# Optimization experiments

Measured on AMD Instinct MI355X. Metric: run time of the kernel, lower is better.

The kernel has to match this reference:

```python
import jax, jax.numpy as jnp
import numpy as np

N_NODES = 50000
N_EDGES = 800000
IN_CH = 128
HID_CH = 128


def setup_inputs() -> dict:
    key = jax.random.key(0)
    k1, k2, k3, k4 = jax.random.split(key, 4)
    x = jax.random.normal(k1, (N_NODES, IN_CH), dtype=jnp.float32)
    edge_index = jax.random.randint(k2, (2, N_EDGES), 0, N_NODES, dtype=jnp.int32)
    # Glorot-ish init for weights
    W1 = jax.random.normal(k3, (IN_CH, HID_CH), dtype=jnp.float32) / np.sqrt(IN_CH)
    b1 = jnp.zeros((HID_CH,), dtype=jnp.float32)
    W2 = jax.random.normal(k4, (HID_CH, 1), dtype=jnp.float32) / np.sqrt(HID_CH)
    b2 = jnp.zeros((1,), dtype=jnp.float32)
    return {"x": x, "edge_index": edge_index, "W1": W1, "b1": b1, "W2": W2, "b2": b2}


def gcn_conv(x, W, b, src, dst, n_nodes):
    """PyG GCNConv: add self-loops, symmetric deg normalization, linear + bias."""
    h = x @ W  # [N, out]
    # degree including self-loop (edge weights are 1)
    deg = jnp.zeros((n_nodes,), dtype=h.dtype).at[dst].add(1.0) + 1.0
    dinv = jax.lax.rsqrt(deg)  # deg >= 1, safe
    norm = dinv[src] * dinv[dst]  # [E]
    msg = h[src] * norm[:, None]  # gather + edgewise scale
    out = jax.ops.segment_sum(msg, dst, num_segments=n_nodes)
    # self-loop contribution: norm_ii = dinv[i]^2
    out = out + h * (dinv * dinv)[:, None]
    return out + b


def reference(x, edge_index, W1, b1, W2, b2):
    src, dst = edge_index[0], edge_index[1]
    n = x.shape[0]
    z = jax.nn.relu(gcn_conv(x, W1, b1, src, dst, n))
    z = gcn_conv(z, W2, b2, src, dst, n)  # [N, 1]
    # decode: edgewise dot product + sigmoid
    logits = jnp.sum(z[src] * z[dst], axis=1)  # [E]
    return jax.nn.sigmoid(logits)
```

## Files before the change

### kernel.cpp

```cpp
#include <hip/hip_runtime.h>
#include <hip/hip_bf16.h>
#include <math.h>

#define N_NODES 50000
#define N_EDGES 800000
#define CH 128
#define WID 64
#define SH 8
#define NBKT 196
#define BCAP 5120

typedef _Float16 half2t __attribute__((ext_vector_type(2)));
typedef _Float16 half4t __attribute__((ext_vector_type(4)));
typedef _Float16 half8t __attribute__((ext_vector_type(8)));
typedef float    floatx4 __attribute__((ext_vector_type(4)));

__global__ void k_zero(int* __restrict__ gcur) {
    gcur[threadIdx.x] = 0;
}

__global__ __launch_bounds__(256) void k_bin(const int* __restrict__ src,
                                             const int* __restrict__ dst,
                                             int* __restrict__ gcur,
                                             unsigned int* __restrict__ pairs,
                                             const float* __restrict__ b1,
                                             const float* __restrict__ W2,
                                             float* __restrict__ b1p,
                                             float* __restrict__ W2p, int E) {
    __shared__ int hist[NBKT];
    __shared__ int gpos[NBKT];
    const int t = threadIdx.x;
    if (t < NBKT) hist[t] = 0;
    __syncthreads();
    const int base = blockIdx.x * 1024;
    int bb[4], rr[4];
    unsigned int vv[4];
#pragma unroll
    for (int i = 0; i < 4; ++i) {
        int e = base + i * 256 + t;
        bb[i] = -1;
        if (e < E) {
            int d = dst[e];
            bb[i] = d >> SH;
            vv[i] = (unsigned int)src[e] | ((unsigned int)(d & 255) << 16);
            rr[i] = atomicAdd(&hist[bb[i]], 1);
        }
    }
    __syncthreads();
    if (t < NBKT) {
        int c = hist[t];
        gpos[t] = (c > 0) ? atomicAdd(&gcur[t], c) : 0;
    }
    __syncthreads();
#pragma unroll
    for (int i = 0; i < 4; ++i) {
        if (bb[i] >= 0) {
            int p = gpos[bb[i]] + rr[i];
            if (p < BCAP) pairs[(size_t)bb[i] * BCAP + p] = vv[i];
        }
    }
    if (blockIdx.x == 0 && t < 128) {
        int cp = t;
        int c  = (cp & 7) * 16 + (cp >> 3);
        b1p[cp] = b1[c];
        W2p[cp] = W2[c];
    }
}

__global__ __launch_bounds__(256) void k_build(const int* __restrict__ gcur,
                                               const unsigned int* __restrict__ pairs,
                                               unsigned short* __restrict__ ell,
                                               int* __restrict__ cnt_g,
                                               float* __restrict__ dinv, int N) {
    __shared__ unsigned short ell_s[256 * WID];
    __shared__ int cnt_s[256];
    const int t = threadIdx.x, b = blockIdx.x;
    cnt_s[t] = 0;
    __syncthreads();
    const int cntb = min(gcur[b], BCAP);
    const unsigned int* pp = pairs + (size_t)b * BCAP;
    for (int j = t; j < cntb; j += 256) {
        unsigned int u = pp[j];
        int lo = u >> 16;
        int c = atomicAdd(&cnt_s[lo], 1);
        if (c < WID) ell_s[lo * WID + c] = (unsigned short)(u & 0xFFFFu);
    }
    __syncthreads();
    const unsigned int* ls = (const unsigned int*)ell_s;
    unsigned int* lg = (unsigned int*)ell + (size_t)b * (256 * WID / 2);
#pragma unroll
    for (int i = 0; i < 32; ++i) lg[t + 256 * i] = ls[t + 256 * i];
    int node = b * 256 + t;
    if (node < N) {
        cnt_g[node] = cnt_s[t];
        dinv[node]  = rsqrtf((float)cnt_s[t] + 1.0f);
    }
}

__global__ __launch_bounds__(256) void k_gemm(const float* __restrict__ x,
                                              const float* __restrict__ W,
                                              const float* __restrict__ dinv,
                                              _Float16* __restrict__ hs, int M) {
    __shared__ _Float16 Wh[32 * 128 * 4];
    const int tid = threadIdx.x;
#pragma unroll
    for (int pass = 0; pass < 16; ++pass) {
        int kg = pass * 2 + (tid >> 7);
        int n  = tid & 127;
        const float* wp = W + (kg * 4) * 128 + n;
        half4t v;
        v[0] = (_Float16)wp[0];
        v[1] = (_Float16)wp[128];
        v[2] = (_Float16)wp[256];
        v[3] = (_Float16)wp[384];
        *(half4t*)&Wh[(kg * 128 + n) * 4] = v;
    }
    __syncthreads();

    const int w    = tid >> 6;
    const int lane = tid & 63;
    const int lrow = lane & 15;
    const int lhi  = lane >> 4;
    const int arow = blockIdx.x * 64 + w * 16 + lrow;
    const bool avalid = arow < M;
    const float* xp = x + (size_t)arow * CH;

    floatx4 acc[8];
#pragma unroll
    for (int t = 0; t < 8; ++t) acc[t] = (floatx4){0.f, 0.f, 0.f, 0.f};

#pragma unroll
    for (int s = 0; s < 8; ++s) {
        floatx4 xa = (floatx4){0.f, 0.f, 0.f, 0.f};
        if (avalid) xa = *(const floatx4*)(xp + s * 16 + lhi * 4);
        half4t a;
        a[0] = (_Float16)xa[0]; a[1] = (_Float16)xa[1];
        a[2] = (_Float16)xa[2]; a[3] = (_Float16)xa[3];
        const int kg = s * 4 + lhi;
#pragma unroll
        for (int t = 0; t < 8; ++t) {
            half4t bv = *(const half4t*)&Wh[(kg * 128 + t * 16 + lrow) * 4];
            acc[t] = __builtin_amdgcn_mfma_f32_16x16x16f16(a, bv, acc[t], 0, 0, 0);
        }
    }

    const int base = blockIdx.x * 64 + w * 16 + lhi * 4;
    if (base < M) {
        floatx4 dv = *(const floatx4*)(dinv + base);
#pragma unroll
        for (int i = 0; i < 4; ++i) {
            half8t o;
#pragma unroll
            for (int t = 0; t < 8; ++t) o[t] = (_Float16)(acc[t][i] * dv[i]);
            *(half8t*)(hs + (size_t)(base + i) * CH + lrow * 8) = o;
        }
    }
}

__global__ __launch_bounds__(256) void k_agg1(const _Float16* __restrict__ hs,
                                              const float* __restrict__ dinv,
                                              const float* __restrict__ b1p,
                                              const float* __restrict__ W2p,
                                              const int* __restrict__ cnt,
                                              const unsigned short* __restrict__ ell,
                                              float* __restrict__ h2s, int N) {
    int node = blockIdx.x * 4 + (threadIdx.x >> 6);
    int lane = threadIdx.x & 63;
    if (node >= N) return;
    int deg = min(cnt[node], WID);
    int l = lane & 15;
    int q = lane >> 4;
    int idxv = (lane < deg) ? (int)ell[(size_t)node * WID + lane] : 0;

    float acc[8];
    if (q == 0) {
        half8t v = *(const half8t*)(hs + (size_t)node * CH + 8 * l);
#pragma unroll
        for (int c = 0; c < 8; ++c) acc[c] = (float)v[c];
    } else {
#pragma unroll
        for (int c = 0; c < 8; ++c) acc[c] = 0.f;
    }

    for (int j0 = q; j0 < deg; j0 += 16) {
        int j1 = j0 + 4, j2 = j0 + 8, j3 = j0 + 12;
        int s0 = __shfl(idxv, j0);
        int s1 = __shfl(idxv, j1 & 63);
        int s2 = __shfl(idxv, j2 & 63);
        int s3 = __shfl(idxv, j3 & 63);
        half8t v0 = *(const half8t*)(hs + (size_t)s0 * CH + 8 * l);
        half8t v1 = *(const half8t*)(hs + (size_t)s1 * CH + 8 * l);
        half8t v2 = *(const half8t*)(hs + (size_t)s2 * CH + 8 * l);
        half8t v3 = *(const half8t*)(hs + (size_t)s3 * CH + 8 * l);
#pragma unroll
        for (int c = 0; c < 8; ++c) acc[c] += (float)v0[c];
        if (j1 < deg) {
#pragma unroll
            for (int c = 0; c < 8; ++c) acc[c] += (float)v1[c];
        }
        if (j2 < deg) {
#pragma unroll
            for (int c = 0; c < 8; ++c) acc[c] += (float)v2[c];
        }
        if (j3 < deg) {
#pragma unroll
            for (int c = 0; c < 8; ++c) acc[c] += (float)v3[c];
        }
    }
#pragma unroll
    for (int c = 0; c < 8; ++c) {
        acc[c] += __shfl_xor(acc[c], 16);
        acc[c] += __shfl_xor(acc[c], 32);
    }

    float di = dinv[node];
    floatx4 b0 = *(const floatx4*)(b1p + 8 * l);
    floatx4 b1v = *(const floatx4*)(b1p + 8 * l + 4);
    floatx4 w0 = *(const floatx4*)(W2p + 8 * l);
    floatx4 w1 = *(const floatx4*)(W2p + 8 * l + 4);
    float a = 0.f;
#pragma unroll
    for (int c = 0; c < 4; ++c) {
        a += fmaxf(fmaf(acc[c], di, b0[c]), 0.f) * w0[c];
        a += fmaxf(fmaf(acc[c + 4], di, b1v[c]), 0.f) * w1[c];
    }
    a += __shfl_down(a, 8);
    a += __shfl_down(a, 4);
    a += __shfl_down(a, 2);
    a += __shfl_down(a, 1);
    if (lane == 0) h2s[node] = a * di;
}

__global__ __launch_bounds__(256) void k_agg2(const float* __restrict__ h2s,
                                              const float* __restrict__ dinv,
                                              const float* __restrict__ b2,
                                              const int* __restrict__ cnt,
                                              const unsigned short* __restrict__ ell,
                                              float* __restrict__ out2, int N) {
    int t = blockIdx.x * blockDim.x + threadIdx.x;
    int node = t >> 3;
    int gl = t & 7;
    if (node >= N) return;
    int deg = min(cnt[node], WID);
    float acc = 0.f;
    for (int j = gl; j < deg; j += 8)
        acc += h2s[ell[(size_t)node * WID + j]];
    acc += __shfl_xor(acc, 4);
    acc += __shfl_xor(acc, 2);
    acc += __shfl_xor(acc, 1);
    if (gl == 0) out2[node] = fmaf(acc + h2s[node], dinv[node], b2[0]);
}

__global__ void k_decode(const float* __restrict__ out2, const int* __restrict__ src,
                         const int* __restrict__ dst, float* __restrict__ out, int E) {
    int t = blockIdx.x * blockDim.x + threadIdx.x;
    int e0 = t * 4;
    if (e0 + 3 < E) {
        int4 s4 = *(const int4*)(src + e0);
        int4 d4 = *(const int4*)(dst + e0);
        float4 o;
        o.x = 1.0f / (1.0f + __expf(-out2[s4.x] * out2[d4.x]));
        o.y = 1.0f / (1.0f + __expf(-out2[s4.y] * out2[d4.y]));
        o.z = 1.0f / (1.0f + __expf(-out2[s4.z] * out2[d4.z]));
        o.w = 1.0f / (1.0f + __expf(-out2[s4.w] * out2[d4.w]));
        *(float4*)(out + e0) = o;
    } else {
        for (int e = e0; e < E; ++e) {
            float z = out2[src[e]] * out2[dst[e]];
            out[e] = 1.0f / (1.0f + __expf(-z));
        }
    }
}

extern "C" void kernel_launch(void* const* d_in, const int* in_sizes, int n_in,
                              void* d_out, int out_size, void* d_ws, size_t ws_size,
                              hipStream_t stream) {
    const float* x   = (const float*)d_in[0];
    const int*   ei  = (const int*)d_in[1];
    const float* W1  = (const float*)d_in[2];
    const float* b1  = (const float*)d_in[3];
    const float* W2  = (const float*)d_in[4];
    const float* b2  = (const float*)d_in[5];
    float* out = (float*)d_out;

    const int N = N_NODES;
    const int E = N_EDGES;
    const int* src = ei;
    const int* dst = ei + E;

    const int NP = 50176;
    float* ws    = (float*)d_ws;
    float* dinv  = ws;
    int*   cnt   = (int*)(ws + NP);
    float* h2s   = ws + 2 * NP;
    float* out2  = ws + 3 * NP;
    float* b1p   = ws + 4 * NP;
    float* W2p   = b1p + CH;
    int*   gcur  = (int*)(W2p + CH);
    unsigned int* pairs = (unsigned int*)(gcur + 256);
    unsigned short* ell = (unsigned short*)(pairs + (size_t)NBKT * BCAP);
    _Float16* hs = (_Float16*)((unsigned int*)ell + (size_t)NP * WID / 2);

    k_zero<<<1, 256, 0, stream>>>(gcur);

    k_bin<<<(E + 1023) / 1024, 256, 0, stream>>>(src, dst, gcur, pairs, b1, W2, b1p, W2p, E);
    k_build<<<NBKT, 256, 0, stream>>>(gcur, pairs, ell, cnt, dinv, N);

    k_gemm<<<(N + 63) / 64, 256, 0, stream>>>(x, W1, dinv, hs, N);

    k_agg1<<<(N + 3) / 4, 256, 0, stream>>>(hs, dinv, b1p, W2p, cnt, ell, h2s, N);
    k_agg2<<<(N * 8 + 255) / 256, 256, 0, stream>>>(h2s, dinv, b2, cnt, ell, out2, N);
    k_decode<<<(E / 4 + 255) / 256, 256, 0, stream>>>(out2, src, dst, out, E);
}
```

Before: 96.20 us.

## Split feature matrix into four channel panels and aggregate each panel separately

The GEMM now writes the fp16 hidden features as four 32-channel panels instead of row-major 128-channel rows. The first-layer aggregation runs four times, once per panel, and combines the partial second-layer dot products through a store on the first pass and atomics after that. Each panel is about 3.2 MB, so the random neighbour gathers should stay in cache. The cost is four kernel launches, reading the neighbour lists four times, and float atomics whose summation order is not fixed. Nontemporal loads and stores are also added to the one-use pair and neighbour-list buffers.

```diff
diff --git a/kernel.cpp b/kernel.cpp
--- a/kernel.cpp
+++ b/kernel.cpp
@@ -9,6 +9,8 @@
 #define SH 8
 #define NBKT 196
 #define BCAP 5120
+#define NPAD 50176
+#define PNL 32
 
 typedef _Float16 half2t __attribute__((ext_vector_type(2)));
 typedef _Float16 half4t __attribute__((ext_vector_type(4)));
@@ -56,7 +58,8 @@
     for (int i = 0; i < 4; ++i) {
         if (bb[i] >= 0) {
             int p = gpos[bb[i]] + rr[i];
-            if (p < BCAP) pairs[(size_t)bb[i] * BCAP + p] = vv[i];
+            if (p < BCAP)
+                __builtin_nontemporal_store(vv[i], pairs + (size_t)bb[i] * BCAP + p);
         }
     }
     if (blockIdx.x == 0 && t < 128) {
@@ -80,7 +83,7 @@
     const int cntb = min(gcur[b], BCAP);
     const unsigned int* pp = pairs + (size_t)b * BCAP;
     for (int j = t; j < cntb; j += 256) {
-        unsigned int u = pp[j];
+        unsigned int u = __builtin_nontemporal_load(pp + j);
         int lo = u >> 16;
         int c = atomicAdd(&cnt_s[lo], 1);
         if (c < WID) ell_s[lo * WID + c] = (unsigned short)(u & 0xFFFFu);
@@ -89,7 +92,8 @@
     const unsigned int* ls = (const unsigned int*)ell_s;
     unsigned int* lg = (unsigned int*)ell + (size_t)b * (256 * WID / 2);
 #pragma unroll
-    for (int i = 0; i < 32; ++i) lg[t + 256 * i] = ls[t + 256 * i];
+    for (int i = 0; i < 32; ++i)
+        __builtin_nontemporal_store(ls[t + 256 * i], lg + t + 256 * i);
     int node = b * 256 + t;
     if (node < N) {
         cnt_g[node] = cnt_s[t];
@@ -100,7 +104,7 @@
 __global__ __launch_bounds__(256) void k_gemm(const float* __restrict__ x,
                                               const float* __restrict__ W,
                                               const float* __restrict__ dinv,
-                                              _Float16* __restrict__ hs, int M) {
+                                              _Float16* __restrict__ hs4, int M) {
     __shared__ _Float16 Wh[32 * 128 * 4];
     const int tid = threadIdx.x;
 #pragma unroll
@@ -147,88 +151,77 @@
     const int base = blockIdx.x * 64 + w * 16 + lhi * 4;
     if (base < M) {
         floatx4 dv = *(const floatx4*)(dinv + base);
+        _Float16* hb = hs4 + (size_t)(lrow >> 2) * NPAD * PNL + (lrow & 3) * 8;
 #pragma unroll
         for (int i = 0; i < 4; ++i) {
             half8t o;
 #pragma unroll
             for (int t = 0; t < 8; ++t) o[t] = (_Float16)(acc[t][i] * dv[i]);
-            *(half8t*)(hs + (size_t)(base + i) * CH + lrow * 8) = o;
-        }
-    }
-}
-
-__global__ __launch_bounds__(256) void k_agg1(const _Float16* __restrict__ hs,
-                                              const float* __restrict__ dinv,
-                                              const float* __restrict__ b1p,
-                                              const float* __restrict__ W2p,
-                                              const int* __restrict__ cnt,
-                                              const unsigned short* __restrict__ ell,
-                                              float* __restrict__ h2s, int N) {
+            *(half8t*)(hb + (size_t)(base + i) * PNL) = o;
+        }
+    }
+}
+
+__global__ __launch_bounds__(256) void k_agg1p(const _Float16* __restrict__ hs4,
+                                               const float* __restrict__ dinv,
+                                               const float* __restrict__ b1p,
+                                               const float* __restrict__ W2p,
+                                               const int* __restrict__ cnt,
+                                               const unsigned short* __restrict__ ell,
+                                               float* __restrict__ h2s, int N,
+                                               int p, int first) {
     int node = blockIdx.x * 4 + (threadIdx.x >> 6);
     int lane = threadIdx.x & 63;
     if (node >= N) return;
     int deg = min(cnt[node], WID);
-    int l = lane & 15;
-    int q = lane >> 4;
-    int idxv = (lane < deg) ? (int)ell[(size_t)node * WID + lane] : 0;
-
-    float acc[8];
-    if (q == 0) {
-        half8t v = *(const half8t*)(hs + (size_t)node * CH + 8 * l);
-#pragma unroll
-        for (int c = 0; c < 8; ++c) acc[c] = (float)v[c];
-    } else {
-#pragma unroll
-        for (int c = 0; c < 8; ++c) acc[c] = 0.f;
-    }
-
-    for (int j0 = q; j0 < deg; j0 += 16) {
-        int j1 = j0 + 4, j2 = j0 + 8, j3 = j0 + 12;
+    int l = lane & 7;
+    int o = lane >> 3;
+    int idxv = (lane < deg)
+        ? (int)__builtin_nontemporal_load(ell + (size_t)node * WID + lane) : 0;
+    const _Float16* hsp = hs4 + (size_t)p * NPAD * PNL;
+
+    float acc[4] = {0.f, 0.f, 0.f, 0.f};
+    if (o == 0) {
+        half4t v = *(const half4t*)(hsp + (size_t)node * PNL + 4 * l);
+#pragma unroll
+        for (int c = 0; c < 4; ++c) acc[c] = (float)v[c];
+    }
+
+    for (int j0 = o; j0 < deg; j0 += 16) {
+        int j1 = j0 + 8;
         int s0 = __shfl(idxv, j0);
         int s1 = __shfl(idxv, j1 & 63);
-        int s2 = __shfl(idxv, j2 & 63);
-        int s3 = __shfl(idxv, j3 & 63);
-        half8t v0 = *(const half8t*)(hs + (size_t)s0 * CH + 8 * l);
-        half8t v1 = *(const half8t*)(hs + (size_t)s1 * CH + 8 * l);
-        half8t v2 = *(const half8t*)(hs + (size_t)s2 * CH + 8 * l);
-        half8t v3 = *(const half8t*)(hs + (size_t)s3 * CH + 8 * l);
-#pragma unroll
-        for (int c = 0; c < 8; ++c) acc[c] += (float)v0[c];
+        half4t v0 = *(const half4t*)(hsp + (size_t)s0 * PNL + 4 * l);
+        half4t v1 = *(const half4t*)(hsp + (size_t)s1 * PNL + 4 * l);
+#pragma unroll
+        for (int c = 0; c < 4; ++c) acc[c] += (float)v0[c];
         if (j1 < deg) {
 #pragma unroll
-            for (int c = 0; c < 8; ++c) acc[c] += (float)v1[c];
-        }
-        if (j2 < deg) {
-#pragma unroll
-            for (int c = 0; c < 8; ++c) acc[c] += (float)v2[c];
-        }
-        if (j3 < deg) {
-#pragma unroll
-            for (int c = 0; c < 8; ++c) acc[c] += (float)v3[c];
-        }
-    }
-#pragma unroll
-    for (int c = 0; c < 8; ++c) {
+            for (int c = 0; c < 4; ++c) acc[c] += (float)v1[c];
+        }
+    }
+#pragma unroll
+    for (int c = 0; c < 4; ++c) {
+        acc[c] += __shfl_xor(acc[c], 8);
         acc[c] += __shfl_xor(acc[c], 16);
         acc[c] += __shfl_xor(acc[c], 32);
     }
 
     float di = dinv[node];
-    floatx4 b0 = *(const floatx4*)(b1p + 8 * l);
-    floatx4 b1v = *(const floatx4*)(b1p + 8 * l + 4);
-    floatx4 w0 = *(const floatx4*)(W2p + 8 * l);
-    floatx4 w1 = *(const floatx4*)(W2p + 8 * l + 4);
+    floatx4 bv = *(const floatx4*)(b1p + p * PNL + 4 * l);
+    floatx4 wv = *(const floatx4*)(W2p + p * PNL + 4 * l);
     float a = 0.f;
 #pragma unroll
-    for (int c = 0; c < 4; ++c) {
-        a += fmaxf(fmaf(acc[c], di, b0[c]), 0.f) * w0[c];
-        a += fmaxf(fmaf(acc[c + 4], di, b1v[c]), 0.f) * w1[c];
-    }
-    a += __shfl_down(a, 8);
+    for (int c = 0; c < 4; ++c)
+        a += fmaxf(fmaf(acc[c], di, bv[c]), 0.f) * wv[c];
     a += __shfl_down(a, 4);
     a += __shfl_down(a, 2);
     a += __shfl_down(a, 1);
-    if (lane == 0) h2s[node] = a * di;
+    if (lane == 0) {
+        float v = a * di;
+        if (first) h2s[node] = v;
+        else       atomicAdd(&h2s[node], v);
+    }
 }
 
 __global__ __launch_bounds__(256) void k_agg2(const float* __restrict__ h2s,
@@ -244,7 +237,7 @@
     int deg = min(cnt[node], WID);
     float acc = 0.f;
     for (int j = gl; j < deg; j += 8)
-        acc += h2s[ell[(size_t)node * WID + j]];
+        acc += h2s[__builtin_nontemporal_load(ell + (size_t)node * WID + j)];
     acc += __shfl_xor(acc, 4);
     acc += __shfl_xor(acc, 2);
     acc += __shfl_xor(acc, 1);
@@ -288,27 +281,28 @@
     const int* src = ei;
     const int* dst = ei + E;
 
-    const int NP = 50176;
     float* ws    = (float*)d_ws;
     float* dinv  = ws;
-    int*   cnt   = (int*)(ws + NP);
-    float* h2s   = ws + 2 * NP;
-    float* out2  = ws + 3 * NP;
-    float* b1p   = ws + 4 * NP;
+    int*   cnt   = (int*)(ws + NPAD);
+    float* h2s   = ws + 2 * NPAD;
+    float* out2  = ws + 3 * NPAD;
+    float* b1p   = ws + 4 * NPAD;
     float* W2p   = b1p + CH;
     int*   gcur  = (int*)(W2p + CH);
     unsigned int* pairs = (unsigned int*)(gcur + 256);
     unsigned short* ell = (unsigned short*)(pairs + (size_t)NBKT * BCAP);
-    _Float16* hs = (_Float16*)((unsigned int*)ell + (size_t)NP * WID / 2);
+    _Float16* hs4 = (_Float16*)((unsigned int*)ell + (size_t)NPAD * WID / 2);
 
     k_zero<<<1, 256, 0, stream>>>(gcur);
 
     k_bin<<<(E + 1023) / 1024, 256, 0, stream>>>(src, dst, gcur, pairs, b1, W2, b1p, W2p, E);
     k_build<<<NBKT, 256, 0, stream>>>(gcur, pairs, ell, cnt, dinv, N);
 
-    k_gemm<<<(N + 63) / 64, 256, 0, stream>>>(x, W1, dinv, hs, N);
-
-    k_agg1<<<(N + 3) / 4, 256, 0, stream>>>(hs, dinv, b1p, W2p, cnt, ell, h2s, N);
+    k_gemm<<<(N + 63) / 64, 256, 0, stream>>>(x, W1, dinv, hs4, N);
+
+    for (int p = 0; p < 4; ++p)
+        k_agg1p<<<(N + 3) / 4, 256, 0, stream>>>(hs4, dinv, b1p, W2p, cnt, ell,
+                                                 h2s, N, p, p == 0 ? 1 : 0);
     k_agg2<<<(N * 8 + 255) / 256, 256, 0, stream>>>(h2s, dinv, b2, cnt, ell, out2, N);
     k_decode<<<(E / 4 + 255) / 256, 256, 0, stream>>>(out2, src, dst, out, E);
 }
```

After: 176.0 us. 1.83x slower.

## Store hidden features as FP8 and gather 16 channels per lane in aggregation

Applied to the files above, without the earlier changes.

The GEMM epilogue now packs the dinv-scaled hidden features into FP8 with cvt_pk_fp8 instead of FP16. This halves the bytes per row that the edge gather in the first aggregation reads. The aggregation kernel is restructured so each lane loads 16 bytes (16 channels) per neighbor, with 8 neighbor slots per wave and an extra shuffle reduction step. The binning kernel also switches to contiguous int4 loads of src and dst. The cost is a large drop in precision for the intermediate features, which risks accuracy against the reference.

```diff
diff --git a/kernel.cpp b/kernel.cpp
--- a/kernel.cpp
+++ b/kernel.cpp
@@ -10,10 +10,10 @@
 #define NBKT 196
 #define BCAP 5120
 
-typedef _Float16 half2t __attribute__((ext_vector_type(2)));
 typedef _Float16 half4t __attribute__((ext_vector_type(4)));
 typedef _Float16 half8t __attribute__((ext_vector_type(8)));
 typedef float    floatx4 __attribute__((ext_vector_type(4)));
+typedef float    floatx2 __attribute__((ext_vector_type(2)));
 
 __global__ void k_zero(int* __restrict__ gcur) {
     gcur[threadIdx.x] = 0;
@@ -32,18 +32,31 @@
     const int t = threadIdx.x;
     if (t < NBKT) hist[t] = 0;
     __syncthreads();
-    const int base = blockIdx.x * 1024;
+    const int e0 = blockIdx.x * 1024 + t * 4;
     int bb[4], rr[4];
     unsigned int vv[4];
-#pragma unroll
-    for (int i = 0; i < 4; ++i) {
-        int e = base + i * 256 + t;
-        bb[i] = -1;
-        if (e < E) {
-            int d = dst[e];
-            bb[i] = d >> SH;
-            vv[i] = (unsigned int)src[e] | ((unsigned int)(d & 255) << 16);
+    if (e0 + 3 < E) {
+        int4 s4 = *(const int4*)(src + e0);
+        int4 d4 = *(const int4*)(dst + e0);
+        int ss[4] = {s4.x, s4.y, s4.z, s4.w};
+        int dd[4] = {d4.x, d4.y, d4.z, d4.w};
+#pragma unroll
+        for (int i = 0; i < 4; ++i) {
+            bb[i] = dd[i] >> SH;
+            vv[i] = (unsigned int)ss[i] | ((unsigned int)(dd[i] & 255) << 16);
             rr[i] = atomicAdd(&hist[bb[i]], 1);
+        }
+    } else {
+#pragma unroll
+        for (int i = 0; i < 4; ++i) {
+            int e = e0 + i;
+            bb[i] = -1;
+            if (e < E) {
+                int d = dst[e];
+                bb[i] = d >> SH;
+                vv[i] = (unsigned int)src[e] | ((unsigned int)(d & 255) << 16);
+                rr[i] = atomicAdd(&hist[bb[i]], 1);
+            }
         }
     }
     __syncthreads();
@@ -100,7 +113,7 @@
 __global__ __launch_bounds__(256) void k_gemm(const float* __restrict__ x,
                                               const float* __restrict__ W,
                                               const float* __restrict__ dinv,
-                                              _Float16* __restrict__ hs, int M) {
+                                              unsigned char* __restrict__ hs8, int M) {
     __shared__ _Float16 Wh[32 * 128 * 4];
     const int tid = threadIdx.x;
 #pragma unroll
@@ -149,82 +162,84 @@
         floatx4 dv = *(const floatx4*)(dinv + base);
 #pragma unroll
         for (int i = 0; i < 4; ++i) {
-            half8t o;
-#pragma unroll
-            for (int t = 0; t < 8; ++t) o[t] = (_Float16)(acc[t][i] * dv[i]);
-            *(half8t*)(hs + (size_t)(base + i) * CH + lrow * 8) = o;
-        }
-    }
-}
-
-__global__ __launch_bounds__(256) void k_agg1(const _Float16* __restrict__ hs,
+            float o[8];
+#pragma unroll
+            for (int t = 0; t < 8; ++t) o[t] = acc[t][i] * dv[i];
+            int w0 = 0, w1 = 0;
+            w0 = __builtin_amdgcn_cvt_pk_fp8_f32(o[0], o[1], w0, false);
+            w0 = __builtin_amdgcn_cvt_pk_fp8_f32(o[2], o[3], w0, true);
+            w1 = __builtin_amdgcn_cvt_pk_fp8_f32(o[4], o[5], w1, false);
+            w1 = __builtin_amdgcn_cvt_pk_fp8_f32(o[6], o[7], w1, true);
+            uint2 st = make_uint2((unsigned int)w0, (unsigned int)w1);
+            *(uint2*)(hs8 + (size_t)(base + i) * CH + lrow * 8) = st;
+        }
+    }
+}
+
+__global__ __launch_bounds__(256) void k_agg1(const unsigned char* __restrict__ hs8,
                                               const float* __restrict__ dinv,
                                               const float* __restrict__ b1p,
                                               const float* __restrict__ W2p,
                                               const int* __restrict__ cnt,
                                               const unsigned short* __restrict__ ell,
                                               float* __restrict__ h2s, int N) {
-    int node = blockIdx.x * 4 + (threadIdx.x >> 6);
-    int lane = threadIdx.x & 63;
+    const int w    = threadIdx.x >> 6;
+    const int lane = threadIdx.x & 63;
+    const int l    = lane & 7;
+    const int o    = lane >> 3;
+    int node = blockIdx.x * 4 + w;
     if (node >= N) return;
     int deg = min(cnt[node], WID);
-    int l = lane & 15;
-    int q = lane >> 4;
     int idxv = (lane < deg) ? (int)ell[(size_t)node * WID + lane] : 0;
 
-    float acc[8];
-    if (q == 0) {
-        half8t v = *(const half8t*)(hs + (size_t)node * CH + 8 * l);
-#pragma unroll
-        for (int c = 0; c < 8; ++c) acc[c] = (float)v[c];
-    } else {
-#pragma unroll
-        for (int c = 0; c < 8; ++c) acc[c] = 0.f;
-    }
-
-    for (int j0 = q; j0 < deg; j0 += 16) {
-        int j1 = j0 + 4, j2 = j0 + 8, j3 = j0 + 12;
+    float acc[16];
+#pragma unroll
+    for (int c = 0; c < 16; ++c) acc[c] = 0.f;
+
+#define ACC_U4(v)  {                                                          \
+        unsigned int ww[4] = {v.x, v.y, v.z, v.w};                            \
+        _Pragma("unroll")                                                     \
+        for (int k = 0; k < 4; ++k) {                                         \
+            floatx2 lo = __builtin_amdgcn_cvt_pk_f32_fp8((int)ww[k], false);  \
+            floatx2 hi = __builtin_amdgcn_cvt_pk_f32_fp8((int)ww[k], true);   \
+            acc[4*k+0] += lo[0]; acc[4*k+1] += lo[1];                         \
+            acc[4*k+2] += hi[0]; acc[4*k+3] += hi[1];                         \
+        }                                                                     \
+    }
+
+    if (o == 0) {
+        uint4 v = *(const uint4*)(hs8 + (size_t)node * CH + 16 * l);
+        ACC_U4(v);
+    }
+
+    for (int j0 = o; j0 < deg; j0 += 16) {
+        int j1 = j0 + 8;
         int s0 = __shfl(idxv, j0);
         int s1 = __shfl(idxv, j1 & 63);
-        int s2 = __shfl(idxv, j2 & 63);
-        int s3 = __shfl(idxv, j3 & 63);
-        half8t v0 = *(const half8t*)(hs + (size_t)s0 * CH + 8 * l);
-        half8t v1 = *(const half8t*)(hs + (size_t)s1 * CH + 8 * l);
-        half8t v2 = *(const half8t*)(hs + (size_t)s2 * CH + 8 * l);
-        half8t v3 = *(const half8t*)(hs + (size_t)s3 * CH + 8 * l);
-#pragma unroll
-        for (int c = 0; c < 8; ++c) acc[c] += (float)v0[c];
-        if (j1 < deg) {
-#pragma unroll
-            for (int c = 0; c < 8; ++c) acc[c] += (float)v1[c];
-        }
-        if (j2 < deg) {
-#pragma unroll
-            for (int c = 0; c < 8; ++c) acc[c] += (float)v2[c];
-        }
-        if (j3 < deg) {
-#pragma unroll
-            for (int c = 0; c < 8; ++c) acc[c] += (float)v3[c];
-        }
-    }
-#pragma unroll
-    for (int c = 0; c < 8; ++c) {
+        uint4 v0 = *(const uint4*)(hs8 + (size_t)s0 * CH + 16 * l);
+        uint4 v1 = *(const uint4*)(hs8 + (size_t)s1 * CH + 16 * l);
+        ACC_U4(v0);
+        if (j1 < deg) ACC_U4(v1);
+    }
+#undef ACC_U4
+
+#pragma unroll
+    for (int c = 0; c < 16; ++c) {
+        acc[c] += __shfl_xor(acc[c], 8);
         acc[c] += __shfl_xor(acc[c], 16);
         acc[c] += __shfl_xor(acc[c], 32);
     }
 
     float di = dinv[node];
-    floatx4 b0 = *(const floatx4*)(b1p + 8 * l);
-    floatx4 b1v = *(const floatx4*)(b1p + 8 * l + 4);
-    floatx4 w0 = *(const floatx4*)(W2p + 8 * l);
-    floatx4 w1 = *(const floatx4*)(W2p + 8 * l + 4);
     float a = 0.f;
 #pragma unroll
-    for (int c = 0; c < 4; ++c) {
-        a += fmaxf(fmaf(acc[c], di, b0[c]), 0.f) * w0[c];
-        a += fmaxf(fmaf(acc[c + 4], di, b1v[c]), 0.f) * w1[c];
-    }
-    a += __shfl_down(a, 8);
+    for (int g = 0; g < 4; ++g) {
+        floatx4 bv = *(const floatx4*)(b1p + 16 * l + 4 * g);
+        floatx4 wv = *(const floatx4*)(W2p + 16 * l + 4 * g);
+#pragma unroll
+        for (int c = 0; c < 4; ++c)
+            a += fmaxf(fmaf(acc[4 * g + c], di, bv[c]), 0.f) * wv[c];
+    }
     a += __shfl_down(a, 4);
     a += __shfl_down(a, 2);
     a += __shfl_down(a, 1);
@@ -299,16 +314,16 @@
     int*   gcur  = (int*)(W2p + CH);
     unsigned int* pairs = (unsigned int*)(gcur + 256);
     unsigned short* ell = (unsigned short*)(pairs + (size_t)NBKT * BCAP);
-    _Float16* hs = (_Float16*)((unsigned int*)ell + (size_t)NP * WID / 2);
+    unsigned char* hs8 = (unsigned char*)((unsigned int*)ell + (size_t)NP * WID / 2);
 
     k_zero<<<1, 256, 0, stream>>>(gcur);
 
     k_bin<<<(E + 1023) / 1024, 256, 0, stream>>>(src, dst, gcur, pairs, b1, W2, b1p, W2p, E);
     k_build<<<NBKT, 256, 0, stream>>>(gcur, pairs, ell, cnt, dinv, N);
 
-    k_gemm<<<(N + 63) / 64, 256, 0, stream>>>(x, W1, dinv, hs, N);
-
-    k_agg1<<<(N + 3) / 4, 256, 0, stream>>>(hs, dinv, b1p, W2p, cnt, ell, h2s, N);
+    k_gemm<<<(N + 63) / 64, 256, 0, stream>>>(x, W1, dinv, hs8, N);
+
+    k_agg1<<<(N + 3) / 4, 256, 0, stream>>>(hs8, dinv, b1p, W2p, cnt, ell, h2s, N);
     k_agg2<<<(N * 8 + 255) / 256, 256, 0, stream>>>(h2s, dinv, b2, cnt, ell, out2, N);
     k_decode<<<(E / 4 + 255) / 256, 256, 0, stream>>>(out2, src, dst, out, E);
 }
```

Result: slower. 99.07 us (+3.0%).
